# Optimization experiments

Hardware: AMD Instinct MI355X
Metric: run time of the kernel (lower is better)

## Reference

```python
import jax, jax.numpy as jnp
import numpy as np

PATCH = 3      # init kwarg patch_size
ALPHA = -1.0   # init kwarg alpha
EPS = 1e-12    # torch F.normalize default eps


def _l2norm(x, axis):
    # matches torch.nn.functional.normalize(p=2): x / max(||x||, eps)
    n = jnp.sqrt(jnp.sum(x * x, axis=axis, keepdims=True))
    return x / jnp.maximum(n, EPS)


def _forward(nbr, ref):
    b, c, h, w = ref.shape
    pad = PATCH // 2
    # ref is detached before being used as the query (ref_clone.detach())
    refn = _l2norm(jax.lax.stop_gradient(ref), axis=1)          # [b,c,h,w], unit over c
    # elementwise reweighting uses ORIGINAL nbr/ref (computed before unfold)
    wdiff = jnp.exp(ALPHA * (nbr - ref) ** 2)                    # [b,c,h,w]
    # reflect-pad + unfold 3x3 neighborhoods; k index is row-major (kh,kw),
    # matching torch unfold's (c, kh, kw) flattening with c kept separate
    npad = jnp.pad(nbr, ((0, 0), (0, 0), (pad, pad), (pad, pad)), mode='reflect')
    patches = jnp.stack(
        [npad[:, :, i:i + h, j:j + w] for i in range(PATCH) for j in range(PATCH)],
        axis=2,
    )                                                            # [b,c,9,h,w]
    patches = _l2norm(patches, axis=1)                           # unit over c per (k,pixel)
    # per-pixel tiny GEMM: [1,c] @ [c,9] -> cosine sims over the 9 neighbors
    d = jnp.einsum('bchw,bckhw->bkhw', refn, patches)            # [b,9,h,w]
    wt = jax.nn.softmax(d, axis=1)                               # softmax over 9 neighbors
    # weighted aggregation of normalized neighbor features
    agg = jnp.einsum('bkhw,bckhw->bchw', wt, patches)            # [b,c,h,w]
    return agg * wdiff


def setup_inputs() -> dict:
    key = jax.random.key(0)
    k1, k2 = jax.random.split(key)
    shape = (2, 64, 256, 256)
    return {
        'nbr': jax.random.normal(k1, shape, dtype=jnp.float32),
        'ref': jax.random.normal(k2, shape, dtype=jnp.float32),
    }


def reference(nbr, ref):
    return _forward(nbr, ref)
```

## Files before the change

kernel.cpp:

```cpp
#include <hip/hip_runtime.h>
#include <stdint.h>


constexpr int C = 64, H = 256, W = 256, HW = H * W;
constexpr int B = 2;

__global__ __launch_bounds__(256, 2) void fused_kernel(const float* __restrict__ nbr,
                                                       const float* __restrict__ ref,
                                                       float* __restrict__ out) {
  __shared__ float buf[10][4][W];

  const int tid  = threadIdx.x;
  const int lane = tid & 63;
  const int wv   = tid >> 6;
  const int x0   = lane * 4;

  const int by = ((blockIdx.x & 7) << 6) | (blockIdx.x >> 3);
  const int b  = by >> 8;
  const int y  = by & 255;
  const int ym = (y == 0)     ? 1     : y - 1;
  const int yp = (y == H - 1) ? H - 2 : y + 1;

  const float* nbase = nbr + (size_t)b * C * HW;
  const float* rrow  = ref + (size_t)b * C * HW + y * W;
  float*       obase = out + (size_t)b * C * HW + y * W;
  const int oM = ym * W, oC = y * W, oP = yp * W;
  const int c0 = wv * 16;

  float dt[4][9], s2[3][6], sr[4];
#pragma unroll
  for (int e = 0; e < 4; ++e) {
    sr[e] = 0.f;
#pragma unroll
    for (int k = 0; k < 9; ++k) dt[e][k] = 0.f;
  }
#pragma unroll
  for (int r = 0; r < 3; ++r)
#pragma unroll
    for (int i = 0; i < 6; ++i) s2[r][i] = 0.f;

#pragma unroll 4
  for (int cc = 0; cc < 16; ++cc) {
    const float* cb = nbase + (size_t)(c0 + cc) * HW;
    const float4 am = *(const float4*)(cb + oM + x0);
    const float4 ac = *(const float4*)(cb + oC + x0);
    const float4 ap = *(const float4*)(cb + oP + x0);
    const float4 rf = *(const float4*)(rrow + (size_t)(c0 + cc) * HW + x0);
    const float rfe[4] = {rf.x, rf.y, rf.z, rf.w};
    sr[0] = fmaf(rfe[0], rfe[0], sr[0]);
    sr[1] = fmaf(rfe[1], rfe[1], sr[1]);
    sr[2] = fmaf(rfe[2], rfe[2], sr[2]);
    sr[3] = fmaf(rfe[3], rfe[3], sr[3]);
    const float4 rows[3] = {am, ac, ap};
#pragma unroll
    for (int r = 0; r < 3; ++r) {
      const float4 v = rows[r];
      float L = __shfl(v.w, lane - 1);
      float R = __shfl(v.x, lane + 1);
      if (lane == 0)  L = v.y;
      if (lane == 63) R = v.z;
      const float win[6] = {L, v.x, v.y, v.z, v.w, R};
#pragma unroll
      for (int i = 0; i < 6; ++i) s2[r][i] = fmaf(win[i], win[i], s2[r][i]);
      const int kb = r * 3;
#pragma unroll
      for (int e = 0; e < 4; ++e)
#pragma unroll
        for (int cx = 0; cx < 3; ++cx)
          dt[e][kb + cx] = fmaf(rfe[e], win[e + cx], dt[e][kb + cx]);
    }
  }

#pragma unroll
  for (int k = 0; k < 9; ++k)
    *(float4*)&buf[k][wv][x0] = float4{dt[0][k], dt[1][k], dt[2][k], dt[3][k]};
  *(float4*)&buf[9][wv][x0] = float4{sr[0], sr[1], sr[2], sr[3]};
  __syncthreads();

  float td[9];
#pragma unroll
  for (int k = 0; k < 9; ++k)
    td[k] = buf[k][0][tid] + buf[k][1][tid] + buf[k][2][tid] + buf[k][3][tid];
  const float tsr = buf[9][0][tid] + buf[9][1][tid] + buf[9][2][tid] + buf[9][3][tid];
  __syncthreads();

#pragma unroll
  for (int k = 0; k < 9; ++k) {
    const int r = k / 3, cx = k % 3;
    *(float4*)&buf[k][wv][x0] = float4{s2[r][cx], s2[r][cx + 1], s2[r][cx + 2], s2[r][cx + 3]};
  }
  __syncthreads();

  float tq[9];
#pragma unroll
  for (int k = 0; k < 9; ++k)
    tq[k] = buf[k][0][tid] + buf[k][1][tid] + buf[k][2][tid] + buf[k][3][tid];

  const float invr = __frsqrt_rn(fmaxf(tsr, 1e-24f));
  float d[9], invp[9];
  float mx = -INFINITY;
#pragma unroll
  for (int k = 0; k < 9; ++k) {
    invp[k] = __frsqrt_rn(fmaxf(tq[k], 1e-24f));
    d[k]    = td[k] * invr * invp[k];
    mx      = fmaxf(mx, d[k]);
  }
  float s = 0.f;
  float cfv[9];
#pragma unroll
  for (int k = 0; k < 9; ++k) {
    cfv[k] = __expf(d[k] - mx);
    s += cfv[k];
  }
  const float sinv = 1.0f / s;

  __syncthreads();
  float* wc = &buf[0][0][0];
#pragma unroll
  for (int k = 0; k < 9; ++k)
    wc[k * W + tid] = cfv[k] * sinv * invp[k];
  __syncthreads();

  float4 cf4[9];
#pragma unroll
  for (int k = 0; k < 9; ++k) cf4[k] = *(const float4*)&wc[k * W + x0];

#pragma unroll 2
  for (int cc = 0; cc < 16; ++cc) {
    const int c = c0 + cc;
    const float* cb = nbase + (size_t)c * HW;
    const float4 am = *(const float4*)(cb + oM + x0);
    const float4 ac = *(const float4*)(cb + oC + x0);
    const float4 ap = *(const float4*)(cb + oP + x0);
    const float4 rf = *(const float4*)(rrow + (size_t)c * HW + x0);

    float agg[4] = {0.f, 0.f, 0.f, 0.f};
    const float4 rows[3] = {am, ac, ap};
#pragma unroll
    for (int r = 0; r < 3; ++r) {
      const float4 v = rows[r];
      float L = __shfl(v.w, lane - 1);
      float R = __shfl(v.x, lane + 1);
      if (lane == 0)  L = v.y;
      if (lane == 63) R = v.z;
      const float win[6] = {L, v.x, v.y, v.z, v.w, R};
#pragma unroll
      for (int cx = 0; cx < 3; ++cx) {
        const float4 cf = cf4[r * 3 + cx];
        const float cfe[4] = {cf.x, cf.y, cf.z, cf.w};
#pragma unroll
        for (int e = 0; e < 4; ++e)
          agg[e] = fmaf(cfe[e], win[e + cx], agg[e]);
      }
    }
    const float ctr[4] = {ac.x, ac.y, ac.z, ac.w};
    const float rfe[4] = {rf.x, rf.y, rf.z, rf.w};
    float oe[4];
#pragma unroll
    for (int e = 0; e < 4; ++e) {
      const float da = ctr[e] - rfe[e];
      oe[e] = agg[e] * __expf(-(da * da));
    }
    float4 o4;
    o4.x = oe[0]; o4.y = oe[1]; o4.z = oe[2]; o4.w = oe[3];
    *(float4*)(obase + (size_t)c * HW + x0) = o4;
  }
}

extern "C" void kernel_launch(void* const* d_in, const int* in_sizes, int n_in,
                              void* d_out, int out_size, void* d_ws, size_t ws_size,
                              hipStream_t stream) {
  const float* nbr = (const float*)d_in[0];
  const float* ref = (const float*)d_in[1];
  float*       out = (float*)d_out;
  fused_kernel<<<dim3(B * H), dim3(256), 0, stream>>>(nbr, ref, out);
}
```

Baseline: 31.32 us.

## Split channels across eight wavefronts per block with two-stage LDS reduction

Doubles the block to 512 threads so each of eight wavefronts handles 8 channels instead of 16 per row. Partial dot products, ref norms and patch sums of squares are folded from the upper four waves into the lower four through shared memory before the existing cross-wave reduction. The aim is more memory-level parallelism and occupancy per row, since each block still covers one image row. The cost is extra LDS round trips and barriers, with half the threads idle during the softmax phase.

```diff
diff --git a/kernel.cpp b/kernel.cpp
--- a/kernel.cpp
+++ b/kernel.cpp
@@ -5,7 +5,7 @@
 constexpr int C = 64, H = 256, W = 256, HW = H * W;
 constexpr int B = 2;
 
-__global__ __launch_bounds__(256, 2) void fused_kernel(const float* __restrict__ nbr,
+__global__ __launch_bounds__(512, 2) void fused_kernel(const float* __restrict__ nbr,
                                                        const float* __restrict__ ref,
                                                        float* __restrict__ out) {
   __shared__ float buf[10][4][W];
@@ -25,7 +25,7 @@
   const float* rrow  = ref + (size_t)b * C * HW + y * W;
   float*       obase = out + (size_t)b * C * HW + y * W;
   const int oM = ym * W, oC = y * W, oP = yp * W;
-  const int c0 = wv * 16;
+  const int c0 = wv * 8;
 
   float dt[4][9], s2[3][6], sr[4];
 #pragma unroll
@@ -40,7 +40,7 @@
     for (int i = 0; i < 6; ++i) s2[r][i] = 0.f;
 
 #pragma unroll 4
-  for (int cc = 0; cc < 16; ++cc) {
+  for (int cc = 0; cc < 8; ++cc) {
     const float* cb = nbase + (size_t)(c0 + cc) * HW;
     const float4 am = *(const float4*)(cb + oM + x0);
     const float4 ac = *(const float4*)(cb + oC + x0);
@@ -71,54 +71,98 @@
     }
   }
 
-#pragma unroll
-  for (int k = 0; k < 9; ++k)
-    *(float4*)&buf[k][wv][x0] = float4{dt[0][k], dt[1][k], dt[2][k], dt[3][k]};
-  *(float4*)&buf[9][wv][x0] = float4{sr[0], sr[1], sr[2], sr[3]};
-  __syncthreads();
-
-  float td[9];
-#pragma unroll
-  for (int k = 0; k < 9; ++k)
-    td[k] = buf[k][0][tid] + buf[k][1][tid] + buf[k][2][tid] + buf[k][3][tid];
-  const float tsr = buf[9][0][tid] + buf[9][1][tid] + buf[9][2][tid] + buf[9][3][tid];
-  __syncthreads();
-
-#pragma unroll
-  for (int k = 0; k < 9; ++k) {
-    const int r = k / 3, cx = k % 3;
-    *(float4*)&buf[k][wv][x0] = float4{s2[r][cx], s2[r][cx + 1], s2[r][cx + 2], s2[r][cx + 3]};
-  }
-  __syncthreads();
-
-  float tq[9];
-#pragma unroll
-  for (int k = 0; k < 9; ++k)
-    tq[k] = buf[k][0][tid] + buf[k][1][tid] + buf[k][2][tid] + buf[k][3][tid];
-
-  const float invr = __frsqrt_rn(fmaxf(tsr, 1e-24f));
-  float d[9], invp[9];
-  float mx = -INFINITY;
-#pragma unroll
-  for (int k = 0; k < 9; ++k) {
-    invp[k] = __frsqrt_rn(fmaxf(tq[k], 1e-24f));
-    d[k]    = td[k] * invr * invp[k];
-    mx      = fmaxf(mx, d[k]);
-  }
-  float s = 0.f;
-  float cfv[9];
-#pragma unroll
-  for (int k = 0; k < 9; ++k) {
-    cfv[k] = __expf(d[k] - mx);
-    s += cfv[k];
-  }
-  const float sinv = 1.0f / s;
-
-  __syncthreads();
+  if (wv >= 4) {
+#pragma unroll
+    for (int k = 0; k < 9; ++k)
+      *(float4*)&buf[k][wv - 4][x0] = float4{dt[0][k], dt[1][k], dt[2][k], dt[3][k]};
+    *(float4*)&buf[9][wv - 4][x0] = float4{sr[0], sr[1], sr[2], sr[3]};
+  }
+  __syncthreads();
+  if (wv < 4) {
+#pragma unroll
+    for (int k = 0; k < 9; ++k) {
+      const float4 t = *(const float4*)&buf[k][wv][x0];
+      dt[0][k] += t.x; dt[1][k] += t.y; dt[2][k] += t.z; dt[3][k] += t.w;
+    }
+    const float4 t9 = *(const float4*)&buf[9][wv][x0];
+    sr[0] += t9.x; sr[1] += t9.y; sr[2] += t9.z; sr[3] += t9.w;
+  }
+  __syncthreads();
+  float* s2b = &buf[0][0][0];
+  if (wv >= 4) {
+    float* p = s2b + ((size_t)((wv - 4) * 64 + lane)) * 18;
+#pragma unroll
+    for (int r = 0; r < 3; ++r)
+#pragma unroll
+      for (int i = 0; i < 6; ++i) p[r * 6 + i] = s2[r][i];
+  }
+  __syncthreads();
+  if (wv < 4) {
+    const float* p = s2b + ((size_t)(wv * 64 + lane)) * 18;
+#pragma unroll
+    for (int r = 0; r < 3; ++r)
+#pragma unroll
+      for (int i = 0; i < 6; ++i) s2[r][i] += p[r * 6 + i];
+  }
+  __syncthreads();
+
+  if (wv < 4) {
+#pragma unroll
+    for (int k = 0; k < 9; ++k)
+      *(float4*)&buf[k][wv][x0] = float4{dt[0][k], dt[1][k], dt[2][k], dt[3][k]};
+    *(float4*)&buf[9][wv][x0] = float4{sr[0], sr[1], sr[2], sr[3]};
+  }
+  __syncthreads();
+  float td[9] = {0,0,0,0,0,0,0,0,0};
+  float tsr = 0.f;
+  if (tid < W) {
+#pragma unroll
+    for (int k = 0; k < 9; ++k)
+      td[k] = buf[k][0][tid] + buf[k][1][tid] + buf[k][2][tid] + buf[k][3][tid];
+    tsr = buf[9][0][tid] + buf[9][1][tid] + buf[9][2][tid] + buf[9][3][tid];
+  }
+  __syncthreads();
+
+  if (wv < 4) {
+#pragma unroll
+    for (int k = 0; k < 9; ++k) {
+      const int r = k / 3, cx = k % 3;
+      *(float4*)&buf[k][wv][x0] = float4{s2[r][cx], s2[r][cx + 1], s2[r][cx + 2], s2[r][cx + 3]};
+    }
+  }
+  __syncthreads();
+  float cfw[9] = {0,0,0,0,0,0,0,0,0};
+  if (tid < W) {
+    float tq[9];
+#pragma unroll
+    for (int k = 0; k < 9; ++k)
+      tq[k] = buf[k][0][tid] + buf[k][1][tid] + buf[k][2][tid] + buf[k][3][tid];
+    const float invr = __frsqrt_rn(fmaxf(tsr, 1e-24f));
+    float d[9], invp[9];
+    float mx = -INFINITY;
+#pragma unroll
+    for (int k = 0; k < 9; ++k) {
+      invp[k] = __frsqrt_rn(fmaxf(tq[k], 1e-24f));
+      d[k]    = td[k] * invr * invp[k];
+      mx      = fmaxf(mx, d[k]);
+    }
+    float s = 0.f;
+#pragma unroll
+    for (int k = 0; k < 9; ++k) {
+      cfw[k] = __expf(d[k] - mx);
+      s += cfw[k];
+    }
+    const float sinv = 1.0f / s;
+#pragma unroll
+    for (int k = 0; k < 9; ++k) cfw[k] *= sinv * invp[k];
+  }
+  __syncthreads();
+
   float* wc = &buf[0][0][0];
-#pragma unroll
-  for (int k = 0; k < 9; ++k)
-    wc[k * W + tid] = cfv[k] * sinv * invp[k];
+  if (tid < W) {
+#pragma unroll
+    for (int k = 0; k < 9; ++k) wc[k * W + tid] = cfw[k];
+  }
   __syncthreads();
 
   float4 cf4[9];
@@ -126,7 +170,7 @@
   for (int k = 0; k < 9; ++k) cf4[k] = *(const float4*)&wc[k * W + x0];
 
 #pragma unroll 2
-  for (int cc = 0; cc < 16; ++cc) {
+  for (int cc = 0; cc < 8; ++cc) {
     const int c = c0 + cc;
     const float* cb = nbase + (size_t)c * HW;
     const float4 am = *(const float4*)(cb + oM + x0);
@@ -173,5 +217,5 @@
   const float* nbr = (const float*)d_in[0];
   const float* ref = (const float*)d_in[1];
   float*       out = (float*)d_out;
-  fused_kernel<<<dim3(B * H), dim3(256), 0, stream>>>(nbr, ref, out);
+  fused_kernel<<<dim3(B * H), dim3(512), 0, stream>>>(nbr, ref, out);
 }
```

New measurement: 31.12 us. Within noise of the previous version (-0.7%).

## Process two output rows per block to share neighbor row loads

Applied to the files above, without the earlier changes.

Each block now computes two adjacent output rows, loading four neighbor rows per channel and reusing the middle two for both outputs' 3x3 windows and norms. This lowers redundant neighbor reads from cache/HBM and halves the grid size. In exchange, register use roughly doubles, launch bounds drop to one block per CU, and the grid shrinks to 256 blocks, reducing latency hiding.

```diff
diff --git a/kernel.cpp b/kernel.cpp
--- a/kernel.cpp
+++ b/kernel.cpp
@@ -5,9 +5,9 @@
 constexpr int C = 64, H = 256, W = 256, HW = H * W;
 constexpr int B = 2;
 
-__global__ __launch_bounds__(256, 2) void fused_kernel(const float* __restrict__ nbr,
-                                                       const float* __restrict__ ref,
-                                                       float* __restrict__ out) {
+__global__ __launch_bounds__(256, 1) void fused2r_kernel(const float* __restrict__ nbr,
+                                                         const float* __restrict__ ref,
+                                                         float* __restrict__ out) {
   __shared__ float buf[10][4][W];
 
   const int tid  = threadIdx.x;
@@ -15,155 +15,235 @@
   const int wv   = tid >> 6;
   const int x0   = lane * 4;
 
-  const int by = ((blockIdx.x & 7) << 6) | (blockIdx.x >> 3);
-  const int b  = by >> 8;
-  const int y  = by & 255;
-  const int ym = (y == 0)     ? 1     : y - 1;
-  const int yp = (y == H - 1) ? H - 2 : y + 1;
+  const int rp = ((blockIdx.x & 7) << 5) | (blockIdx.x >> 3);
+  const int b  = rp >> 7;
+  const int y0 = (rp & 127) * 2;
+  const int ym  = (y0 == 0)     ? 1     : y0 - 1;
+  const int yp2 = (y0 == H - 2) ? H - 2 : y0 + 2;
 
   const float* nbase = nbr + (size_t)b * C * HW;
-  const float* rrow  = ref + (size_t)b * C * HW + y * W;
-  float*       obase = out + (size_t)b * C * HW + y * W;
-  const int oM = ym * W, oC = y * W, oP = yp * W;
+  const float* rrowA = ref + (size_t)b * C * HW + y0 * W;
+  const float* rrowB = rrowA + W;
+  float*       obaseA = out + (size_t)b * C * HW + y0 * W;
+  float*       obaseB = obaseA + W;
+  const int off4[4] = {ym * W, y0 * W, (y0 + 1) * W, yp2 * W};
   const int c0 = wv * 16;
 
-  float dt[4][9], s2[3][6], sr[4];
+  float dtA[4][9], dtB[4][9], s2r[4][6], srA[4], srB[4];
 #pragma unroll
   for (int e = 0; e < 4; ++e) {
-    sr[e] = 0.f;
-#pragma unroll
-    for (int k = 0; k < 9; ++k) dt[e][k] = 0.f;
-  }
-#pragma unroll
-  for (int r = 0; r < 3; ++r)
-#pragma unroll
-    for (int i = 0; i < 6; ++i) s2[r][i] = 0.f;
-
-#pragma unroll 4
+    srA[e] = 0.f; srB[e] = 0.f;
+#pragma unroll
+    for (int k = 0; k < 9; ++k) { dtA[e][k] = 0.f; dtB[e][k] = 0.f; }
+  }
+#pragma unroll
+  for (int rr = 0; rr < 4; ++rr)
+#pragma unroll
+    for (int i = 0; i < 6; ++i) s2r[rr][i] = 0.f;
+
+#pragma unroll 2
   for (int cc = 0; cc < 16; ++cc) {
     const float* cb = nbase + (size_t)(c0 + cc) * HW;
-    const float4 am = *(const float4*)(cb + oM + x0);
-    const float4 ac = *(const float4*)(cb + oC + x0);
-    const float4 ap = *(const float4*)(cb + oP + x0);
-    const float4 rf = *(const float4*)(rrow + (size_t)(c0 + cc) * HW + x0);
-    const float rfe[4] = {rf.x, rf.y, rf.z, rf.w};
-    sr[0] = fmaf(rfe[0], rfe[0], sr[0]);
-    sr[1] = fmaf(rfe[1], rfe[1], sr[1]);
-    sr[2] = fmaf(rfe[2], rfe[2], sr[2]);
-    sr[3] = fmaf(rfe[3], rfe[3], sr[3]);
-    const float4 rows[3] = {am, ac, ap};
-#pragma unroll
-    for (int r = 0; r < 3; ++r) {
-      const float4 v = rows[r];
+    const float4 r0 = *(const float4*)(cb + off4[0] + x0);
+    const float4 r1 = *(const float4*)(cb + off4[1] + x0);
+    const float4 r2 = *(const float4*)(cb + off4[2] + x0);
+    const float4 r3 = *(const float4*)(cb + off4[3] + x0);
+    const float4 fA = *(const float4*)(rrowA + (size_t)(c0 + cc) * HW + x0);
+    const float4 fB = *(const float4*)(rrowB + (size_t)(c0 + cc) * HW + x0);
+    const float feA[4] = {fA.x, fA.y, fA.z, fA.w};
+    const float feB[4] = {fB.x, fB.y, fB.z, fB.w};
+#pragma unroll
+    for (int e = 0; e < 4; ++e) {
+      srA[e] = fmaf(feA[e], feA[e], srA[e]);
+      srB[e] = fmaf(feB[e], feB[e], srB[e]);
+    }
+    const float4 rows[4] = {r0, r1, r2, r3};
+#pragma unroll
+    for (int rr = 0; rr < 4; ++rr) {
+      const float4 v = rows[rr];
       float L = __shfl(v.w, lane - 1);
       float R = __shfl(v.x, lane + 1);
       if (lane == 0)  L = v.y;
       if (lane == 63) R = v.z;
       const float win[6] = {L, v.x, v.y, v.z, v.w, R};
 #pragma unroll
-      for (int i = 0; i < 6; ++i) s2[r][i] = fmaf(win[i], win[i], s2[r][i]);
-      const int kb = r * 3;
-#pragma unroll
-      for (int e = 0; e < 4; ++e)
-#pragma unroll
-        for (int cx = 0; cx < 3; ++cx)
-          dt[e][kb + cx] = fmaf(rfe[e], win[e + cx], dt[e][kb + cx]);
-    }
-  }
-
-#pragma unroll
-  for (int k = 0; k < 9; ++k)
-    *(float4*)&buf[k][wv][x0] = float4{dt[0][k], dt[1][k], dt[2][k], dt[3][k]};
-  *(float4*)&buf[9][wv][x0] = float4{sr[0], sr[1], sr[2], sr[3]};
-  __syncthreads();
-
-  float td[9];
-#pragma unroll
-  for (int k = 0; k < 9; ++k)
-    td[k] = buf[k][0][tid] + buf[k][1][tid] + buf[k][2][tid] + buf[k][3][tid];
-  const float tsr = buf[9][0][tid] + buf[9][1][tid] + buf[9][2][tid] + buf[9][3][tid];
+      for (int i = 0; i < 6; ++i) s2r[rr][i] = fmaf(win[i], win[i], s2r[rr][i]);
+      if (rr < 3) {
+        const int kb = rr * 3;
+#pragma unroll
+        for (int e = 0; e < 4; ++e)
+#pragma unroll
+          for (int cx = 0; cx < 3; ++cx)
+            dtA[e][kb + cx] = fmaf(feA[e], win[e + cx], dtA[e][kb + cx]);
+      }
+      if (rr > 0) {
+        const int kb = (rr - 1) * 3;
+#pragma unroll
+        for (int e = 0; e < 4; ++e)
+#pragma unroll
+          for (int cx = 0; cx < 3; ++cx)
+            dtB[e][kb + cx] = fmaf(feB[e], win[e + cx], dtB[e][kb + cx]);
+      }
+    }
+  }
+
+#pragma unroll
+  for (int k = 0; k < 9; ++k)
+    *(float4*)&buf[k][wv][x0] = float4{dtA[0][k], dtA[1][k], dtA[2][k], dtA[3][k]};
+  *(float4*)&buf[9][wv][x0] = float4{srA[0], srA[1], srA[2], srA[3]};
+  __syncthreads();
+  float tdA[9];
+#pragma unroll
+  for (int k = 0; k < 9; ++k)
+    tdA[k] = buf[k][0][tid] + buf[k][1][tid] + buf[k][2][tid] + buf[k][3][tid];
+  const float tsrA = buf[9][0][tid] + buf[9][1][tid] + buf[9][2][tid] + buf[9][3][tid];
   __syncthreads();
 
 #pragma unroll
   for (int k = 0; k < 9; ++k) {
     const int r = k / 3, cx = k % 3;
-    *(float4*)&buf[k][wv][x0] = float4{s2[r][cx], s2[r][cx + 1], s2[r][cx + 2], s2[r][cx + 3]};
-  }
-  __syncthreads();
-
-  float tq[9];
-#pragma unroll
-  for (int k = 0; k < 9; ++k)
-    tq[k] = buf[k][0][tid] + buf[k][1][tid] + buf[k][2][tid] + buf[k][3][tid];
-
-  const float invr = __frsqrt_rn(fmaxf(tsr, 1e-24f));
-  float d[9], invp[9];
-  float mx = -INFINITY;
-#pragma unroll
-  for (int k = 0; k < 9; ++k) {
-    invp[k] = __frsqrt_rn(fmaxf(tq[k], 1e-24f));
-    d[k]    = td[k] * invr * invp[k];
-    mx      = fmaxf(mx, d[k]);
-  }
-  float s = 0.f;
-  float cfv[9];
-#pragma unroll
-  for (int k = 0; k < 9; ++k) {
-    cfv[k] = __expf(d[k] - mx);
-    s += cfv[k];
-  }
-  const float sinv = 1.0f / s;
-
-  __syncthreads();
+    *(float4*)&buf[k][wv][x0] = float4{s2r[r][cx], s2r[r][cx + 1], s2r[r][cx + 2], s2r[r][cx + 3]};
+  }
+  __syncthreads();
+  float cfvA[9];
+  {
+    float tq[9];
+#pragma unroll
+    for (int k = 0; k < 9; ++k)
+      tq[k] = buf[k][0][tid] + buf[k][1][tid] + buf[k][2][tid] + buf[k][3][tid];
+    const float invr = __frsqrt_rn(fmaxf(tsrA, 1e-24f));
+    float d[9], invp[9];
+    float mx = -INFINITY;
+#pragma unroll
+    for (int k = 0; k < 9; ++k) {
+      invp[k] = __frsqrt_rn(fmaxf(tq[k], 1e-24f));
+      d[k]    = tdA[k] * invr * invp[k];
+      mx      = fmaxf(mx, d[k]);
+    }
+    float s = 0.f;
+#pragma unroll
+    for (int k = 0; k < 9; ++k) { cfvA[k] = __expf(d[k] - mx); s += cfvA[k]; }
+    const float sinv = 1.0f / s;
+#pragma unroll
+    for (int k = 0; k < 9; ++k) cfvA[k] *= sinv * invp[k];
+  }
+  __syncthreads();
+
+#pragma unroll
+  for (int k = 0; k < 9; ++k)
+    *(float4*)&buf[k][wv][x0] = float4{dtB[0][k], dtB[1][k], dtB[2][k], dtB[3][k]};
+  *(float4*)&buf[9][wv][x0] = float4{srB[0], srB[1], srB[2], srB[3]};
+  __syncthreads();
+  float tdB[9];
+#pragma unroll
+  for (int k = 0; k < 9; ++k)
+    tdB[k] = buf[k][0][tid] + buf[k][1][tid] + buf[k][2][tid] + buf[k][3][tid];
+  const float tsrB = buf[9][0][tid] + buf[9][1][tid] + buf[9][2][tid] + buf[9][3][tid];
+  __syncthreads();
+
+#pragma unroll
+  for (int k = 0; k < 9; ++k) {
+    const int r = k / 3 + 1, cx = k % 3;
+    *(float4*)&buf[k][wv][x0] = float4{s2r[r][cx], s2r[r][cx + 1], s2r[r][cx + 2], s2r[r][cx + 3]};
+  }
+  __syncthreads();
+  float cfvB[9];
+  {
+    float tq[9];
+#pragma unroll
+    for (int k = 0; k < 9; ++k)
+      tq[k] = buf[k][0][tid] + buf[k][1][tid] + buf[k][2][tid] + buf[k][3][tid];
+    const float invr = __frsqrt_rn(fmaxf(tsrB, 1e-24f));
+    float d[9], invp[9];
+    float mx = -INFINITY;
+#pragma unroll
+    for (int k = 0; k < 9; ++k) {
+      invp[k] = __frsqrt_rn(fmaxf(tq[k], 1e-24f));
+      d[k]    = tdB[k] * invr * invp[k];
+      mx      = fmaxf(mx, d[k]);
+    }
+    float s = 0.f;
+#pragma unroll
+    for (int k = 0; k < 9; ++k) { cfvB[k] = __expf(d[k] - mx); s += cfvB[k]; }
+    const float sinv = 1.0f / s;
+#pragma unroll
+    for (int k = 0; k < 9; ++k) cfvB[k] *= sinv * invp[k];
+  }
+  __syncthreads();
+
   float* wc = &buf[0][0][0];
 #pragma unroll
-  for (int k = 0; k < 9; ++k)
-    wc[k * W + tid] = cfv[k] * sinv * invp[k];
-  __syncthreads();
-
-  float4 cf4[9];
-#pragma unroll
-  for (int k = 0; k < 9; ++k) cf4[k] = *(const float4*)&wc[k * W + x0];
+  for (int k = 0; k < 9; ++k) {
+    wc[k * W + tid]       = cfvA[k];
+    wc[(9 + k) * W + tid] = cfvB[k];
+  }
+  __syncthreads();
+
+  float4 cfA[9], cfB[9];
+#pragma unroll
+  for (int k = 0; k < 9; ++k) {
+    cfA[k] = *(const float4*)&wc[k * W + x0];
+    cfB[k] = *(const float4*)&wc[(9 + k) * W + x0];
+  }
 
 #pragma unroll 2
   for (int cc = 0; cc < 16; ++cc) {
     const int c = c0 + cc;
     const float* cb = nbase + (size_t)c * HW;
-    const float4 am = *(const float4*)(cb + oM + x0);
-    const float4 ac = *(const float4*)(cb + oC + x0);
-    const float4 ap = *(const float4*)(cb + oP + x0);
-    const float4 rf = *(const float4*)(rrow + (size_t)c * HW + x0);
-
-    float agg[4] = {0.f, 0.f, 0.f, 0.f};
-    const float4 rows[3] = {am, ac, ap};
-#pragma unroll
-    for (int r = 0; r < 3; ++r) {
-      const float4 v = rows[r];
+    const float4 r0 = *(const float4*)(cb + off4[0] + x0);
+    const float4 r1 = *(const float4*)(cb + off4[1] + x0);
+    const float4 r2 = *(const float4*)(cb + off4[2] + x0);
+    const float4 r3 = *(const float4*)(cb + off4[3] + x0);
+    const float4 fA = *(const float4*)(rrowA + (size_t)c * HW + x0);
+    const float4 fB = *(const float4*)(rrowB + (size_t)c * HW + x0);
+
+    float aggA[4] = {0.f, 0.f, 0.f, 0.f};
+    float aggB[4] = {0.f, 0.f, 0.f, 0.f};
+    const float4 rows[4] = {r0, r1, r2, r3};
+#pragma unroll
+    for (int rr = 0; rr < 4; ++rr) {
+      const float4 v = rows[rr];
       float L = __shfl(v.w, lane - 1);
       float R = __shfl(v.x, lane + 1);
       if (lane == 0)  L = v.y;
       if (lane == 63) R = v.z;
       const float win[6] = {L, v.x, v.y, v.z, v.w, R};
-#pragma unroll
-      for (int cx = 0; cx < 3; ++cx) {
-        const float4 cf = cf4[r * 3 + cx];
-        const float cfe[4] = {cf.x, cf.y, cf.z, cf.w};
-#pragma unroll
-        for (int e = 0; e < 4; ++e)
-          agg[e] = fmaf(cfe[e], win[e + cx], agg[e]);
-      }
-    }
-    const float ctr[4] = {ac.x, ac.y, ac.z, ac.w};
-    const float rfe[4] = {rf.x, rf.y, rf.z, rf.w};
-    float oe[4];
+      if (rr < 3) {
+#pragma unroll
+        for (int cx = 0; cx < 3; ++cx) {
+          const float4 cf = cfA[rr * 3 + cx];
+          const float cfe[4] = {cf.x, cf.y, cf.z, cf.w};
+#pragma unroll
+          for (int e = 0; e < 4; ++e) aggA[e] = fmaf(cfe[e], win[e + cx], aggA[e]);
+        }
+      }
+      if (rr > 0) {
+#pragma unroll
+        for (int cx = 0; cx < 3; ++cx) {
+          const float4 cf = cfB[(rr - 1) * 3 + cx];
+          const float cfe[4] = {cf.x, cf.y, cf.z, cf.w};
+#pragma unroll
+          for (int e = 0; e < 4; ++e) aggB[e] = fmaf(cfe[e], win[e + cx], aggB[e]);
+        }
+      }
+    }
+    const float ctrA[4] = {r1.x, r1.y, r1.z, r1.w};
+    const float ctrB[4] = {r2.x, r2.y, r2.z, r2.w};
+    const float feA[4]  = {fA.x, fA.y, fA.z, fA.w};
+    const float feB[4]  = {fB.x, fB.y, fB.z, fB.w};
+    float oA[4], oB[4];
 #pragma unroll
     for (int e = 0; e < 4; ++e) {
-      const float da = ctr[e] - rfe[e];
-      oe[e] = agg[e] * __expf(-(da * da));
-    }
-    float4 o4;
-    o4.x = oe[0]; o4.y = oe[1]; o4.z = oe[2]; o4.w = oe[3];
-    *(float4*)(obase + (size_t)c * HW + x0) = o4;
+      const float dA = ctrA[e] - feA[e];
+      const float dB = ctrB[e] - feB[e];
+      oA[e] = aggA[e] * __expf(-(dA * dA));
+      oB[e] = aggB[e] * __expf(-(dB * dB));
+    }
+    float4 o4A, o4B;
+    o4A.x = oA[0]; o4A.y = oA[1]; o4A.z = oA[2]; o4A.w = oA[3];
+    o4B.x = oB[0]; o4B.y = oB[1]; o4B.z = oB[2]; o4B.w = oB[3];
+    *(float4*)(obaseA + (size_t)c * HW + x0) = o4A;
+    *(float4*)(obaseB + (size_t)c * HW + x0) = o4B;
   }
 }
 
@@ -173,5 +253,5 @@
   const float* nbr = (const float*)d_in[0];
   const float* ref = (const float*)d_in[1];
   float*       out = (float*)d_out;
-  fused_kernel<<<dim3(B * H), dim3(256), 0, stream>>>(nbr, ref, out);
+  fused2r_kernel<<<dim3(B * H / 2), dim3(256), 0, stream>>>(nbr, ref, out);
 }
```

Measured after the change: 33.17 us. 1.06x slower.

## Split fused kernel into partial, reduce and apply kernels via workspace

Applied to the files above, without the earlier changes.

Replaces the single fused per-row kernel with three launches. The first computes per-quarter channel partial dot products and norms into a workspace, the second reduces them and computes softmax coefficients, and the third applies the weighted aggregation with many more blocks spread across channel pairs. The aim is more parallelism and better occupancy than 512 large blocks with shared-memory reductions. In exchange it adds heavy workspace traffic (about 76 planes of pixel data written and read), two extra launches, and a second read of nbr and ref. It falls back to the fused kernel when the workspace is too small.

```diff
diff --git a/kernel.cpp b/kernel.cpp
--- a/kernel.cpp
+++ b/kernel.cpp
@@ -3,29 +3,26 @@
 
 
 constexpr int C = 64, H = 256, W = 256, HW = H * W;
-constexpr int B = 2;
-
-__global__ __launch_bounds__(256, 2) void fused_kernel(const float* __restrict__ nbr,
-                                                       const float* __restrict__ ref,
-                                                       float* __restrict__ out) {
-  __shared__ float buf[10][4][W];
-
-  const int tid  = threadIdx.x;
-  const int lane = tid & 63;
-  const int wv   = tid >> 6;
+constexpr int B = 2, PIX = B * HW;
+
+__global__ __launch_bounds__(64) void partial_kernel(const float* __restrict__ nbr,
+                                                     const float* __restrict__ ref,
+                                                     float* __restrict__ ws) {
+  const int lane = threadIdx.x;
   const int x0   = lane * 4;
 
-  const int by = ((blockIdx.x & 7) << 6) | (blockIdx.x >> 3);
-  const int b  = by >> 8;
-  const int y  = by & 255;
+  const int bid = ((blockIdx.x & 7) << 8) | (blockIdx.x >> 3);
+  const int q   = bid & 3;
+  const int by  = bid >> 2;
+  const int b   = by >> 8;
+  const int y   = by & 255;
   const int ym = (y == 0)     ? 1     : y - 1;
   const int yp = (y == H - 1) ? H - 2 : y + 1;
 
   const float* nbase = nbr + (size_t)b * C * HW;
   const float* rrow  = ref + (size_t)b * C * HW + y * W;
-  float*       obase = out + (size_t)b * C * HW + y * W;
   const int oM = ym * W, oC = y * W, oP = yp * W;
-  const int c0 = wv * 16;
+  const int c0 = q * 16;
 
   float dt[4][9], s2[3][6], sr[4];
 #pragma unroll
@@ -71,6 +68,206 @@
     }
   }
 
+  const int base = by * W + x0;
+#pragma unroll
+  for (int k = 0; k < 9; ++k)
+    *(float4*)&ws[(size_t)(q * 19 + k) * PIX + base] = float4{dt[0][k], dt[1][k], dt[2][k], dt[3][k]};
+#pragma unroll
+  for (int k = 0; k < 9; ++k) {
+    const int r = k / 3, cx = k % 3;
+    *(float4*)&ws[(size_t)(q * 19 + 9 + k) * PIX + base] =
+        float4{s2[r][cx], s2[r][cx + 1], s2[r][cx + 2], s2[r][cx + 3]};
+  }
+  *(float4*)&ws[(size_t)(q * 19 + 18) * PIX + base] = float4{sr[0], sr[1], sr[2], sr[3]};
+}
+
+__global__ __launch_bounds__(256) void reduce_kernel(float* __restrict__ ws) {
+  const int tid = threadIdx.x;
+  const int by  = ((blockIdx.x & 7) << 6) | (blockIdx.x >> 3);
+  const int pix = by * W + tid;
+
+  float td[9], tq[9];
+#pragma unroll
+  for (int k = 0; k < 9; ++k) {
+    td[k] = ws[(size_t)(0 * 19 + k) * PIX + pix] + ws[(size_t)(1 * 19 + k) * PIX + pix]
+          + ws[(size_t)(2 * 19 + k) * PIX + pix] + ws[(size_t)(3 * 19 + k) * PIX + pix];
+    tq[k] = ws[(size_t)(0 * 19 + 9 + k) * PIX + pix] + ws[(size_t)(1 * 19 + 9 + k) * PIX + pix]
+          + ws[(size_t)(2 * 19 + 9 + k) * PIX + pix] + ws[(size_t)(3 * 19 + 9 + k) * PIX + pix];
+  }
+  const float tsr = ws[(size_t)(0 * 19 + 18) * PIX + pix] + ws[(size_t)(1 * 19 + 18) * PIX + pix]
+                  + ws[(size_t)(2 * 19 + 18) * PIX + pix] + ws[(size_t)(3 * 19 + 18) * PIX + pix];
+
+  const float invr = __frsqrt_rn(fmaxf(tsr, 1e-24f));
+  float d[9], invp[9];
+  float mx = -INFINITY;
+#pragma unroll
+  for (int k = 0; k < 9; ++k) {
+    invp[k] = __frsqrt_rn(fmaxf(tq[k], 1e-24f));
+    d[k]    = td[k] * invr * invp[k];
+    mx      = fmaxf(mx, d[k]);
+  }
+  float s = 0.f;
+  float cfv[9];
+#pragma unroll
+  for (int k = 0; k < 9; ++k) {
+    cfv[k] = __expf(d[k] - mx);
+    s += cfv[k];
+  }
+  const float sinv = 1.0f / s;
+#pragma unroll
+  for (int k = 0; k < 9; ++k)
+    ws[(size_t)k * PIX + pix] = cfv[k] * sinv * invp[k];
+}
+
+__global__ __launch_bounds__(256) void apply_kernel(const float* __restrict__ nbr,
+                                                    const float* __restrict__ ref,
+                                                    const float* __restrict__ coef,
+                                                    float* __restrict__ out) {
+  const int blk  = ((blockIdx.x & 7) << 9) | (blockIdx.x >> 3);
+  const int gid  = blk * 256 + threadIdx.x;
+  const int lane = gid & 63;
+  const int x0   = lane * 4;
+  const int t    = gid >> 6;
+  const int y    = t & 255;
+  const int u    = t >> 8;
+  const int b    = u >> 5;
+  const int c0   = (u & 31) * 2;
+
+  const int ym = (y == 0)     ? 1     : y - 1;
+  const int yp = (y == H - 1) ? H - 2 : y + 1;
+
+  const float* n0  = nbr + ((size_t)b * C + c0) * HW;
+  const float* n1  = n0 + HW;
+  const float* r0p = ref + ((size_t)b * C + c0) * HW;
+  float*       o0  = out + ((size_t)b * C + c0) * HW;
+
+  const float4 a0 = *(const float4*)(n0 + ym * W + x0);
+  const float4 a1 = *(const float4*)(n0 + y  * W + x0);
+  const float4 a2 = *(const float4*)(n0 + yp * W + x0);
+  const float4 b0 = *(const float4*)(n1 + ym * W + x0);
+  const float4 b1 = *(const float4*)(n1 + y  * W + x0);
+  const float4 b2 = *(const float4*)(n1 + yp * W + x0);
+  const float4 f0 = *(const float4*)(r0p + y * W + x0);
+  const float4 f1 = *(const float4*)(r0p + HW + y * W + x0);
+
+  float La0 = __shfl(a0.w, lane - 1), Ra0 = __shfl(a0.x, lane + 1);
+  float La1 = __shfl(a1.w, lane - 1), Ra1 = __shfl(a1.x, lane + 1);
+  float La2 = __shfl(a2.w, lane - 1), Ra2 = __shfl(a2.x, lane + 1);
+  float Lb0 = __shfl(b0.w, lane - 1), Rb0 = __shfl(b0.x, lane + 1);
+  float Lb1 = __shfl(b1.w, lane - 1), Rb1 = __shfl(b1.x, lane + 1);
+  float Lb2 = __shfl(b2.w, lane - 1), Rb2 = __shfl(b2.x, lane + 1);
+  if (lane == 0)  { La0 = a0.y; La1 = a1.y; La2 = a2.y; Lb0 = b0.y; Lb1 = b1.y; Lb2 = b2.y; }
+  if (lane == 63) { Ra0 = a0.z; Ra1 = a1.z; Ra2 = a2.z; Rb0 = b0.z; Rb1 = b1.z; Rb2 = b2.z; }
+
+  float va[3][6] = {{La0, a0.x, a0.y, a0.z, a0.w, Ra0},
+                    {La1, a1.x, a1.y, a1.z, a1.w, Ra1},
+                    {La2, a2.x, a2.y, a2.z, a2.w, Ra2}};
+  float vb[3][6] = {{Lb0, b0.x, b0.y, b0.z, b0.w, Rb0},
+                    {Lb1, b1.x, b1.y, b1.z, b1.w, Rb1},
+                    {Lb2, b2.x, b2.y, b2.z, b2.w, Rb2}};
+
+  const int cbase = b * HW + y * W + x0;
+  float aga[4] = {0.f, 0.f, 0.f, 0.f};
+  float agb[4] = {0.f, 0.f, 0.f, 0.f};
+#pragma unroll
+  for (int k = 0; k < 9; ++k) {
+    const float4 cf = *(const float4*)(coef + (size_t)k * PIX + cbase);
+    const int r  = k / 3;
+    const int cx = k % 3;
+    const float cfe[4] = {cf.x, cf.y, cf.z, cf.w};
+#pragma unroll
+    for (int e = 0; e < 4; ++e) {
+      aga[e] = fmaf(cfe[e], va[r][e + cx], aga[e]);
+      agb[e] = fmaf(cfe[e], vb[r][e + cx], agb[e]);
+    }
+  }
+
+  const float ctra[4] = {a1.x, a1.y, a1.z, a1.w};
+  const float ctrb[4] = {b1.x, b1.y, b1.z, b1.w};
+  const float rfa[4]  = {f0.x, f0.y, f0.z, f0.w};
+  const float rfb[4]  = {f1.x, f1.y, f1.z, f1.w};
+  float oae[4], obe[4];
+#pragma unroll
+  for (int e = 0; e < 4; ++e) {
+    const float da = ctra[e] - rfa[e];
+    const float db = ctrb[e] - rfb[e];
+    oae[e] = aga[e] * __expf(-(da * da));
+    obe[e] = agb[e] * __expf(-(db * db));
+  }
+  float4 oa, ob4;
+  oa.x = oae[0]; oa.y = oae[1]; oa.z = oae[2]; oa.w = oae[3];
+  ob4.x = obe[0]; ob4.y = obe[1]; ob4.z = obe[2]; ob4.w = obe[3];
+
+  *(float4*)(o0 + y * W + x0) = oa;
+  *(float4*)(o0 + HW + y * W + x0) = ob4;
+}
+
+__global__ __launch_bounds__(256, 2) void fused_kernel(const float* __restrict__ nbr,
+                                                       const float* __restrict__ ref,
+                                                       float* __restrict__ out) {
+  __shared__ float buf[10][4][W];
+
+  const int tid  = threadIdx.x;
+  const int lane = tid & 63;
+  const int wv   = tid >> 6;
+  const int x0   = lane * 4;
+
+  const int by = ((blockIdx.x & 7) << 6) | (blockIdx.x >> 3);
+  const int b  = by >> 8;
+  const int y  = by & 255;
+  const int ym = (y == 0)     ? 1     : y - 1;
+  const int yp = (y == H - 1) ? H - 2 : y + 1;
+
+  const float* nbase = nbr + (size_t)b * C * HW;
+  const float* rrow  = ref + (size_t)b * C * HW + y * W;
+  float*       obase = out + (size_t)b * C * HW + y * W;
+  const int oM = ym * W, oC = y * W, oP = yp * W;
+  const int c0 = wv * 16;
+
+  float dt[4][9], s2[3][6], sr[4];
+#pragma unroll
+  for (int e = 0; e < 4; ++e) {
+    sr[e] = 0.f;
+#pragma unroll
+    for (int k = 0; k < 9; ++k) dt[e][k] = 0.f;
+  }
+#pragma unroll
+  for (int r = 0; r < 3; ++r)
+#pragma unroll
+    for (int i = 0; i < 6; ++i) s2[r][i] = 0.f;
+
+#pragma unroll 4
+  for (int cc = 0; cc < 16; ++cc) {
+    const float* cb = nbase + (size_t)(c0 + cc) * HW;
+    const float4 am = *(const float4*)(cb + oM + x0);
+    const float4 ac = *(const float4*)(cb + oC + x0);
+    const float4 ap = *(const float4*)(cb + oP + x0);
+    const float4 rf = *(const float4*)(rrow + (size_t)(c0 + cc) * HW + x0);
+    const float rfe[4] = {rf.x, rf.y, rf.z, rf.w};
+    sr[0] = fmaf(rfe[0], rfe[0], sr[0]);
+    sr[1] = fmaf(rfe[1], rfe[1], sr[1]);
+    sr[2] = fmaf(rfe[2], rfe[2], sr[2]);
+    sr[3] = fmaf(rfe[3], rfe[3], sr[3]);
+    const float4 rows[3] = {am, ac, ap};
+#pragma unroll
+    for (int r = 0; r < 3; ++r) {
+      const float4 v = rows[r];
+      float L = __shfl(v.w, lane - 1);
+      float R = __shfl(v.x, lane + 1);
+      if (lane == 0)  L = v.y;
+      if (lane == 63) R = v.z;
+      const float win[6] = {L, v.x, v.y, v.z, v.w, R};
+#pragma unroll
+      for (int i = 0; i < 6; ++i) s2[r][i] = fmaf(win[i], win[i], s2[r][i]);
+      const int kb = r * 3;
+#pragma unroll
+      for (int e = 0; e < 4; ++e)
+#pragma unroll
+        for (int cx = 0; cx < 3; ++cx)
+          dt[e][kb + cx] = fmaf(rfe[e], win[e + cx], dt[e][kb + cx]);
+    }
+  }
+
 #pragma unroll
   for (int k = 0; k < 9; ++k)
     *(float4*)&buf[k][wv][x0] = float4{dt[0][k], dt[1][k], dt[2][k], dt[3][k]};
@@ -173,5 +370,14 @@
   const float* nbr = (const float*)d_in[0];
   const float* ref = (const float*)d_in[1];
   float*       out = (float*)d_out;
-  fused_kernel<<<dim3(B * H), dim3(256), 0, stream>>>(nbr, ref, out);
-}
+  const size_t need = (size_t)4 * 19 * PIX * sizeof(float);
+
+  if (ws_size >= need) {
+    float* ws = (float*)d_ws;
+    partial_kernel<<<dim3(2048), dim3(64), 0, stream>>>(nbr, ref, ws);
+    reduce_kernel<<<dim3(512), dim3(256), 0, stream>>>(ws);
+    apply_kernel<<<dim3(PIX / 4 * (C / 2) / 256), dim3(256), 0, stream>>>(nbr, ref, ws, out);
+  } else {
+    fused_kernel<<<dim3(B * H), dim3(256), 0, stream>>>(nbr, ref, out);
+  }
+}
```

New measurement: 52.49 us. +67.6%, slower.
